# Optimization experiments

Hardware: AMD Instinct MI355X
Metric: run time of the kernel (lower is better)

Reference implementation:

```python
import jax, jax.numpy as jnp
import numpy as np

N_NODES = 50000
N_EDGES = 800000
IN_DIM = 128
HID = 256
OUT = 256


def setup_inputs() -> dict:
    key = jax.random.key(0)
    ks = jax.random.split(key, 16)
    s = 0.05
    return {
        "x": jax.random.normal(ks[0], (N_NODES, IN_DIM), jnp.float32),
        "edge_index": jax.random.randint(ks[1], (2, N_EDGES), 0, N_NODES),
        "W_gcn": jax.random.normal(ks[2], (IN_DIM, HID), jnp.float32) * s,
        "b_gcn": jnp.zeros((HID,), jnp.float32),
        "W_gat": jax.random.normal(ks[3], (IN_DIM, HID), jnp.float32) * s,
        "att_src": jax.random.normal(ks[4], (HID,), jnp.float32) * s,
        "att_dst": jax.random.normal(ks[5], (HID,), jnp.float32) * s,
        "b_gat": jnp.zeros((HID,), jnp.float32),
        "W_sage_l": jax.random.normal(ks[6], (IN_DIM, HID), jnp.float32) * s,
        "b_sage_l": jnp.zeros((HID,), jnp.float32),
        "W_sage_r": jax.random.normal(ks[7], (IN_DIM, HID), jnp.float32) * s,
        "W_fus": jax.random.normal(ks[8], (3 * HID, OUT), jnp.float32) * s,
        "b_fus": jnp.zeros((OUT,), jnp.float32),
    }


def reference(x, edge_index, W_gcn, b_gcn, W_gat, att_src, att_dst, b_gat,
              W_sage_l, b_sage_l, W_sage_r, W_fus, b_fus):
    N = x.shape[0]
    row, col = edge_index[0], edge_index[1]  # source -> target
    loop = jnp.arange(N)
    row_sl = jnp.concatenate([row, loop])  # with self-loops (GCN & GAT)
    col_sl = jnp.concatenate([col, loop])

    # ---- GCNConv: symmetric normalization, transform-then-propagate ----
    xg = x @ W_gcn  # [N, H]
    w = jnp.ones(row_sl.shape[0], x.dtype)
    deg = jax.ops.segment_sum(w, col_sl, num_segments=N)  # >= 1 due to self-loops
    dis = jax.lax.rsqrt(deg)
    norm = dis[row_sl] * dis[col_sl]  # [E+N]
    h_gcn = jax.ops.segment_sum(norm[:, None] * xg[row_sl], col_sl, num_segments=N) + b_gcn

    # ---- GATConv (1 head): attention softmax over incoming edges ----
    xa = x @ W_gat  # [N, H]
    a_src = xa @ att_src  # [N]
    a_dst = xa @ att_dst  # [N]
    e = jax.nn.leaky_relu(a_src[row_sl] + a_dst[col_sl], 0.2)  # [E+N]
    m = jax.ops.segment_max(e, col_sl, num_segments=N)  # per-target max (stable softmax)
    p = jnp.exp(e - m[col_sl])
    z = jax.ops.segment_sum(p, col_sl, num_segments=N)
    alpha = p / (z[col_sl] + 1e-16)
    h_gat = jax.ops.segment_sum(alpha[:, None] * xa[row_sl], col_sl, num_segments=N) + b_gat

    # ---- SAGEConv: mean neighbor aggregation (no self-loops) + root ----
    msum = jax.ops.segment_sum(x[row], col, num_segments=N)
    cnt = jax.ops.segment_sum(jnp.ones(row.shape[0], x.dtype), col, num_segments=N)
    mean = msum / jnp.maximum(cnt, 1.0)[:, None]
    h_sage = mean @ W_sage_l + b_sage_l + x @ W_sage_r

    h = jnp.concatenate([jax.nn.relu(h_gcn), jax.nn.relu(h_gat), jax.nn.relu(h_sage)], axis=1)
    return h @ W_fus + b_fus
```

## Files before the change

### kernel.cpp

```cpp
#include <hip/hip_runtime.h>
#include <hip/hip_bf16.h>

typedef __hip_bfloat16 bf16;
typedef short bf16x8 __attribute__((ext_vector_type(8)));
typedef float f32x4  __attribute__((ext_vector_type(4)));

static constexpr int D_IN  = 128;
static constexpr int D_H   = 256;
static constexpr int D_CAT = 768;

__device__ __forceinline__ float lrelu(float v){ return v > 0.f ? v : 0.2f*v; }
__device__ __forceinline__ bf16  f2b(float v){ return __float2bfloat16(v); }
__device__ __forceinline__ unsigned packb(float lo, float hi){
  bf16 a = f2b(lo), b = f2b(hi);
  unsigned short ua, ub;
  __builtin_memcpy(&ua, &a, 2); __builtin_memcpy(&ub, &b, 2);
  return (unsigned)ua | ((unsigned)ub << 16);
}
__device__ __forceinline__ short bbits(float v){
  bf16 h = f2b(v); short s; __builtin_memcpy(&s, &h, 2); return s;
}
__device__ __forceinline__ unsigned fenc(float f){
  unsigned u = __float_as_uint(f);
  return (u & 0x80000000u) ? ~u : (u | 0x80000000u);
}
__device__ __forceinline__ float fdec(unsigned e){
  unsigned u = (e & 0x80000000u) ? (e ^ 0x80000000u) : ~e;
  return __uint_as_float(u);
}

__device__ __forceinline__ void gload_lds16(const void* g, void* l){
  __builtin_amdgcn_global_load_lds(
      (const __attribute__((address_space(1))) unsigned*)g,
      (__attribute__((address_space(3))) unsigned*)l, 16, 0, 0);
}

__global__ __launch_bounds__(256) void k_prep(
    const float* __restrict__ Wg, const float* __restrict__ Wa,
    const float* __restrict__ Wl, const float* __restrict__ Wr,
    const float* __restrict__ Wf,
    const float* __restrict__ att_src, const float* __restrict__ att_dst,
    const float* __restrict__ bg, const float* __restrict__ ba,
    const float* __restrict__ bs,
    const int* __restrict__ ecol,
    bf16* __restrict__ W1t, bf16* __restrict__ W2t,
    float* __restrict__ bias1, float* __restrict__ wsrc,
    float* __restrict__ wdst, int* __restrict__ cnt, int E)
{
  int b = blockIdx.x, t = threadIdx.x;
  if (b < 768){
    int n = b, k = t;
    float v = 0.f;
    if (n < 256)      { if (k < 128)  v = Wg[(size_t)k*D_H + n]; }
    else if (n < 512) { if (k >= 128) v = Wa[(size_t)(k-128)*D_H + (n-256)]; }
    else              { v = (k < 128) ? Wl[(size_t)k*D_H + (n-512)]
                                      : Wr[(size_t)(k-128)*D_H + (n-512)]; }
    W1t[(size_t)n*256 + k] = f2b(v);
  } else if (b < 1024){
    int n = b - 768;
    for (int k = t; k < D_CAT; k += 256)
      W2t[(size_t)n*D_CAT + k] = f2b(Wf[(size_t)k*D_H + n]);
  } else if (b == 1024){
    bias1[t] = bg[t]; bias1[256+t] = ba[t]; bias1[512+t] = bs[t];
  } else if (b == 1025){
    if (t < 128){
      float s1 = 0.f, s2 = 0.f;
      for (int j = 0; j < D_H; ++j){
        float w = Wa[(size_t)t*D_H + j];
        s1 = fmaf(w, att_src[j], s1);
        s2 = fmaf(w, att_dst[j], s2);
      }
      wsrc[t] = s1; wdst[t] = s2;
    }
  } else {
    int e = (b - 1026)*256 + t;
    if (e < E) atomicAdd(&cnt[ecol[e]], 1);
  }
}

__global__ __launch_bounds__(256) void k_asrc(const float* __restrict__ x,
                                              const float* __restrict__ wsrc,
                                              const float* __restrict__ wdst,
                                              bf16* __restrict__ xb,
                                              float* __restrict__ a_src,
                                              float* __restrict__ a_dst,
                                              unsigned* __restrict__ maxenc,
                                              int N){
  int w = threadIdx.x >> 6, l = threadIdx.x & 63;
  int c = blockIdx.x*4 + w;
  if (c >= N) return;
  float2 xv = *(const float2*)(x + (size_t)c*D_IN + 2*l);
  *(unsigned*)(xb + (size_t)c*D_IN + 2*l) = packb(xv.x, xv.y);
  float s1 = xv.x*wsrc[2*l] + xv.y*wsrc[2*l+1];
  float s2 = xv.x*wdst[2*l] + xv.y*wdst[2*l+1];
  #pragma unroll
  for (int o = 32; o > 0; o >>= 1){
    s1 += __shfl_down(s1, o);
    s2 += __shfl_down(s2, o);
  }
  if (l == 0){ a_src[c] = s1; a_dst[c] = s2; maxenc[c] = fenc(s1); }
}

__global__ __launch_bounds__(256) void k_scanA(const int* __restrict__ cnt,
                                               int* __restrict__ indptr,
                                               int* __restrict__ bsum,
                                               float* __restrict__ dis, int N){
  __shared__ int s[256];
  int t = threadIdx.x, i = blockIdx.x*256 + t;
  int v = (i < N) ? cnt[i] : 0;
  s[t] = v; __syncthreads();
  #pragma unroll
  for (int d = 1; d < 256; d <<= 1){
    int tmp = (t >= d) ? s[t-d] : 0;
    __syncthreads();
    s[t] += tmp;
    __syncthreads();
  }
  if (i < N){
    indptr[i] = s[t] - v;
    dis[i] = rsqrtf((float)v + 1.0f);
  }
  if (t == 255) bsum[blockIdx.x] = s[255];
}

__global__ __launch_bounds__(256) void k_scanB(const int* __restrict__ bsum,
                                               int* __restrict__ boff,
                                               int* __restrict__ indptr,
                                               int nb, int N, int E){
  __shared__ int s[256];
  int t = threadIdx.x;
  int v = (t < nb) ? bsum[t] : 0;
  s[t] = v; __syncthreads();
  #pragma unroll
  for (int d = 1; d < 256; d <<= 1){
    int tmp = (t >= d) ? s[t-d] : 0;
    __syncthreads();
    s[t] += tmp;
    __syncthreads();
  }
  boff[t] = s[t] - v;
  if (t == 0) indptr[N] = E;
}

__global__ __launch_bounds__(256) void k_scanC(int* __restrict__ indptr,
                                               const int* __restrict__ boff, int N){
  int i = blockIdx.x*256 + threadIdx.x;
  if (i < N) indptr[i] += boff[blockIdx.x];
}

__global__ __launch_bounds__(256) void k_fill(const int* __restrict__ row,
                                              const int* __restrict__ col,
                                              const int* __restrict__ indptr,
                                              int* __restrict__ cursor,
                                              int* __restrict__ esrc,
                                              const float* __restrict__ a_src,
                                              unsigned* __restrict__ maxenc,
                                              int E){
  int e = blockIdx.x*256 + threadIdx.x;
  if (e < E){
    int r = row[e], c = col[e];
    int p = indptr[c] + atomicAdd(&cursor[c], 1);
    esrc[p] = r;
    atomicMax(&maxenc[c], fenc(a_src[r]));
  }
}

__global__ __launch_bounds__(256) void k_aggx(
    const int* __restrict__ indptr, const int* __restrict__ esrc,
    const bf16* __restrict__ xb,
    const float* __restrict__ a_src, const float* __restrict__ a_dst,
    const float* __restrict__ dis,
    const unsigned* __restrict__ maxenc,
    bf16* __restrict__ AGG, int N)
{
  int c = blockIdx.x;
  if (c >= N) return;
  int t = threadIdx.x;
  int beg = indptr[c], end = indptr[c+1];
  int deg = end - beg;
  float adst = a_dst[c], dc = dis[c];
  float eself = lrelu(a_src[c] + adst);
  float m = lrelu(fdec(maxenc[c]) + adst);

  __shared__ int   s_src[256];
  __shared__ float s_pe[256];
  __shared__ float s_ds[256];
  __shared__ float pg[4][128], pa[4][128], ps[4][128];
  __shared__ float red[4];

  float p0 = __expf(eself - m);
  float z_loc = (t == 0) ? p0 : 0.f;

  int d2 = t & 63;
  int g  = t >> 6;
  float g0=0.f,g1=0.f,a0=0.f,a1=0.f,sg0=0.f,sg1=0.f;

  for (int ch0 = beg; ch0 < end; ch0 += 256){
    int n = min(256, end - ch0);
    __syncthreads();
    if (t < n){
      int s = esrc[ch0 + t];
      float pe = __expf(lrelu(a_src[s] + adst) - m);
      s_src[t] = s; s_pe[t] = pe; s_ds[t] = dis[s];
      z_loc += pe;
    }
    __syncthreads();
    int i = g;
    for (; i + 28 < n; i += 32){
      unsigned u[8]; float pe[8], ds[8];
      #pragma unroll
      for (int q = 0; q < 8; ++q){
        int s = s_src[i + 4*q];
        u[q] = *(const unsigned*)(xb + (size_t)s*D_IN + 2*d2);
      }
      #pragma unroll
      for (int q = 0; q < 8; ++q){ pe[q] = s_pe[i+4*q]; ds[q] = s_ds[i+4*q]; }
      #pragma unroll
      for (int q = 0; q < 8; ++q){
        float x0 = __uint_as_float(u[q] << 16);
        float x1 = __uint_as_float(u[q] & 0xffff0000u);
        g0 = fmaf(ds[q], x0, g0); g1 = fmaf(ds[q], x1, g1);
        a0 = fmaf(pe[q], x0, a0); a1 = fmaf(pe[q], x1, a1);
        sg0 += x0; sg1 += x1;
      }
    }
    for (; i < n; i += 4){
      int s = s_src[i];
      float pe = s_pe[i], ds = s_ds[i];
      unsigned u = *(const unsigned*)(xb + (size_t)s*D_IN + 2*d2);
      float x0 = __uint_as_float(u << 16);
      float x1 = __uint_as_float(u & 0xffff0000u);
      g0 = fmaf(ds, x0, g0); g1 = fmaf(ds, x1, g1);
      a0 = fmaf(pe, x0, a0); a1 = fmaf(pe, x1, a1);
      sg0 += x0; sg1 += x1;
    }
  }

  #pragma unroll
  for (int o = 32; o > 0; o >>= 1) z_loc += __shfl_down(z_loc, o);
  if ((t & 63) == 0) red[t >> 6] = z_loc;
  __syncthreads();
  float z = red[0] + red[1] + red[2] + red[3];

  pg[g][2*d2] = g0; pg[g][2*d2+1] = g1;
  pa[g][2*d2] = a0; pa[g][2*d2+1] = a1;
  ps[g][2*d2] = sg0; ps[g][2*d2+1] = sg1;
  __syncthreads();

  if (t < 64){
    int d0 = 2*t, d1 = 2*t + 1;
    float G0 = pg[0][d0]+pg[1][d0]+pg[2][d0]+pg[3][d0];
    float G1 = pg[0][d1]+pg[1][d1]+pg[2][d1]+pg[3][d1];
    float A0 = pa[0][d0]+pa[1][d0]+pa[2][d0]+pa[3][d0];
    float A1 = pa[0][d1]+pa[1][d1]+pa[2][d1]+pa[3][d1];
    float S0 = ps[0][d0]+ps[1][d0]+ps[2][d0]+ps[3][d0];
    float S1 = ps[0][d1]+ps[1][d1]+ps[2][d1]+ps[3][d1];
    unsigned xu = *(const unsigned*)(xb + (size_t)c*D_IN + d0);
    float xc0 = __uint_as_float(xu << 16);
    float xc1 = __uint_as_float(xu & 0xffff0000u);
    float invz = 1.f / (z + 1e-16f);
    float invc = 1.f / fmaxf((float)deg, 1.f);
    unsigned* rowp = (unsigned*)(AGG + (size_t)c*512);
    rowp[t]        = packb(dc*(G0 + dc*xc0), dc*(G1 + dc*xc1));
    rowp[64 + t]   = packb((A0 + p0*xc0)*invz, (A1 + p0*xc1)*invz);
    rowp[128 + t]  = packb(S0*invc, S1*invc);
    rowp[192 + t]  = xu;
  }
}

__global__ __launch_bounds__(512, 4) void k_mlp(
    const bf16* __restrict__ AGG,
    const bf16* __restrict__ W1t,
    const bf16* __restrict__ W2t,
    const float* __restrict__ bias1,
    const float* __restrict__ bias2,
    float* __restrict__ out, int M)
{
  __shared__ short A_res[4*64*64];
  __shared__ short Hc[2*64*64];
  __shared__ short SW[256*64];
  int tid  = threadIdx.x;
  int bm   = blockIdx.x*64;
  int wave = tid >> 6, lane = tid & 63;
  int l15  = lane & 15, l4 = lane >> 4;
  int wr   = (wave >> 2)*32;
  int wcol = wave & 3;

  f32x4 oacc[2][4] = {};

  #pragma unroll
  for (int i = 0; i < 4; ++i){
    int slot = i*512 + tid;
    int rr = (slot >> 3) & 63, gp = slot & 7;
    int gk = gp ^ (rr & 7);
    int p  = slot >> 9;
    int row = bm + rr; if (row >= M) row = M - 1;
    gload_lds16(AGG + (size_t)row*512 + p*64 + gk*8, A_res + (size_t)slot*8);
  }

  #pragma unroll
  for (int j = 0; j < 6; ++j){
    if (j == 4){
      #pragma unroll
      for (int i = 0; i < 4; ++i){
        int slot = i*512 + tid;
        int rr = (slot >> 3) & 63, gp = slot & 7;
        int gk = gp ^ (rr & 7);
        int p  = slot >> 9;
        int row = bm + rr; if (row >= M) row = M - 1;
        gload_lds16(AGG + (size_t)row*512 + 256 + p*64 + gk*8, A_res + (size_t)slot*8);
      }
    }
    const int p0 = (j < 2) ? 0 : ((j < 4) ? 2 : 0);
    const int np = (j < 4) ? 2 : 4;
    f32x4 hacc[2][2] = {};
    for (int pp = 0; pp < np; ++pp){
      int p = p0 + pp;
      __syncthreads();
      #pragma unroll
      for (int i = 0; i < 2; ++i){
        int slot = i*512 + tid;
        int r = slot >> 3, gp = slot & 7;
        int gk = gp ^ (r & 7);
        gload_lds16(W1t + (size_t)(j*128 + r)*256 + p*64 + gk*8, SW + (size_t)slot*8);
      }
      __syncthreads();
      #pragma unroll
      for (int kk = 0; kk < 2; ++kk){
        bf16x8 af[2], bfv[2];
        #pragma unroll
        for (int mi = 0; mi < 2; ++mi){
          int r = wr + mi*16 + l15;
          int gk = kk*4 + l4;
          af[mi] = *(const bf16x8*)(A_res + p*4096 + r*64 + ((gk ^ (r & 7))*8));
        }
        #pragma unroll
        for (int ni = 0; ni < 2; ++ni){
          int r = wcol*32 + ni*16 + l15;
          int gk = kk*4 + l4;
          bfv[ni] = *(const bf16x8*)(SW + r*64 + ((gk ^ (r & 7))*8));
        }
        #pragma unroll
        for (int mi = 0; mi < 2; ++mi)
          #pragma unroll
          for (int ni = 0; ni < 2; ++ni)
            hacc[mi][ni] = __builtin_amdgcn_mfma_f32_16x16x32_bf16(
                               af[mi], bfv[ni], hacc[mi][ni], 0, 0, 0);
      }
    }
    #pragma unroll
    for (int mi = 0; mi < 2; ++mi)
      #pragma unroll
      for (int ni = 0; ni < 2; ++ni){
        int cc = wcol*32 + ni*16 + l15;
        float bb = bias1[j*128 + cc];
        int q = cc >> 6, g8 = (cc >> 3) & 7, e = cc & 7;
        #pragma unroll
        for (int r = 0; r < 4; ++r){
          int rr = wr + mi*16 + l4*4 + r;
          float v = fmaxf(hacc[mi][ni][r] + bb, 0.f);
          Hc[q*4096 + rr*64 + ((g8 ^ (rr & 7))*8) + e] = bbits(v);
        }
      }
    #pragma unroll
    for (int q = 0; q < 2; ++q){
      __syncthreads();
      #pragma unroll
      for (int i = 0; i < 4; ++i){
        int slot = i*512 + tid;
        int r = slot >> 3, gp = slot & 7;
        int gk = gp ^ (r & 7);
        gload_lds16(W2t + (size_t)r*768 + j*128 + q*64 + gk*8, SW + (size_t)slot*8);
      }
      __syncthreads();
      #pragma unroll
      for (int kk = 0; kk < 2; ++kk){
        bf16x8 af[2], bfv[4];
        #pragma unroll
        for (int mi = 0; mi < 2; ++mi){
          int r = wr + mi*16 + l15;
          int gk = kk*4 + l4;
          af[mi] = *(const bf16x8*)(Hc + q*4096 + r*64 + ((gk ^ (r & 7))*8));
        }
        #pragma unroll
        for (int ni = 0; ni < 4; ++ni){
          int r = wcol*64 + ni*16 + l15;
          int gk = kk*4 + l4;
          bfv[ni] = *(const bf16x8*)(SW + r*64 + ((gk ^ (r & 7))*8));
        }
        #pragma unroll
        for (int mi = 0; mi < 2; ++mi)
          #pragma unroll
          for (int ni = 0; ni < 4; ++ni)
            oacc[mi][ni] = __builtin_amdgcn_mfma_f32_16x16x32_bf16(
                               af[mi], bfv[ni], oacc[mi][ni], 0, 0, 0);
      }
    }
  }

  #pragma unroll
  for (int mi = 0; mi < 2; ++mi)
    #pragma unroll
    for (int r = 0; r < 4; ++r){
      int row = bm + wr + mi*16 + l4*4 + r;
      if (row >= M) continue;
      #pragma unroll
      for (int ni = 0; ni < 4; ++ni){
        int col = wcol*64 + ni*16 + l15;
        out[(size_t)row*256 + col] = oacc[mi][ni][r] + bias2[col];
      }
    }
}

static inline char* carve(char*& p, size_t bytes){
  char* r = p;
  p += (bytes + 255) & ~(size_t)255;
  return r;
}

extern "C" void kernel_launch(void* const* d_in, const int* in_sizes, int n_in,
                              void* d_out, int out_size, void* d_ws, size_t ws_size,
                              hipStream_t stream) {
  const float* x        = (const float*)d_in[0];
  const int*   ei       = (const int*)  d_in[1];
  const float* W_gcn    = (const float*)d_in[2];
  const float* b_gcn    = (const float*)d_in[3];
  const float* W_gat    = (const float*)d_in[4];
  const float* att_src  = (const float*)d_in[5];
  const float* att_dst  = (const float*)d_in[6];
  const float* b_gat    = (const float*)d_in[7];
  const float* W_sage_l = (const float*)d_in[8];
  const float* b_sage_l = (const float*)d_in[9];
  const float* W_sage_r = (const float*)d_in[10];
  const float* W_fus    = (const float*)d_in[11];
  const float* b_fus    = (const float*)d_in[12];

  const int N = in_sizes[0] / D_IN;
  const int E = in_sizes[1] / 2;
  const int* erow = ei;
  const int* ecol = ei + E;

  char* p = (char*)d_ws;
  bf16*     AGG    = (bf16*)    carve(p, (size_t)N*512*2);
  bf16*     xb     = (bf16*)    carve(p, (size_t)N*D_IN*2);
  bf16*     W1t    = (bf16*)    carve(p, (size_t)D_CAT*256*2);
  bf16*     W2t    = (bf16*)    carve(p, (size_t)256*D_CAT*2);
  float*    bias1  = (float*)   carve(p, D_CAT*4);
  float*    wsrc   = (float*)   carve(p, D_IN*4);
  float*    wdst   = (float*)   carve(p, D_IN*4);
  float*    a_src  = (float*)   carve(p, (size_t)N*4);
  float*    a_dst  = (float*)   carve(p, (size_t)N*4);
  float*    dis    = (float*)   carve(p, (size_t)N*4);
  unsigned* maxenc = (unsigned*)carve(p, (size_t)N*4);
  int*      cnt    = (int*)     carve(p, (size_t)N*4);
  int*      cursor = (int*)     carve(p, (size_t)N*4);
  int*      indptr = (int*)     carve(p, (size_t)(N+1)*4);
  int*      bsum   = (int*)     carve(p, 256*4);
  int*      boff   = (int*)     carve(p, 256*4);
  int*      esrc   = (int*)     carve(p, (size_t)E*4);
  (void)ws_size; (void)n_in; (void)out_size;

  hipMemsetAsync(cnt,    0, (size_t)N*4, stream);
  hipMemsetAsync(cursor, 0, (size_t)N*4, stream);

  const int nb = (N + 255) / 256;
  const int eb = (E + 255) / 256;

  k_prep<<<1026 + eb, 256, 0, stream>>>(W_gcn, W_gat, W_sage_l, W_sage_r, W_fus,
                                        att_src, att_dst, b_gcn, b_gat, b_sage_l,
                                        ecol, W1t, W2t, bias1, wsrc, wdst, cnt, E);

  k_asrc<<<(N + 3)/4, 256, 0, stream>>>(x, wsrc, wdst, xb, a_src, a_dst,
                                        maxenc, N);

  k_scanA<<<nb, 256, 0, stream>>>(cnt, indptr, bsum, dis, N);
  k_scanB<<<1, 256, 0, stream>>>(bsum, boff, indptr, nb, N, E);
  k_scanC<<<nb, 256, 0, stream>>>(indptr, boff, N);
  k_fill <<<eb, 256, 0, stream>>>(erow, ecol, indptr, cursor, esrc,
                                  a_src, maxenc, E);

  k_aggx<<<N, 256, 0, stream>>>(indptr, esrc, xb, a_src, a_dst, dis,
                                maxenc, AGG, N);

  k_mlp<<<(N + 63)/64, 512, 0, stream>>>(AGG, W1t, W2t, bias1, b_fus,
                                         (float*)d_out, N);
}
```

Baseline: 392.8 us.

## Assign one wavefront per target node in aggregation kernel

Measured after the change: 338.2 us. 1.16x faster.

```diff
diff --git a/kernel.cpp b/kernel.cpp
--- a/kernel.cpp
+++ b/kernel.cpp
@@ -173,48 +173,43 @@
     const unsigned* __restrict__ maxenc,
     bf16* __restrict__ AGG, int N)
 {
-  int c = blockIdx.x;
+  int w = threadIdx.x >> 6, l = threadIdx.x & 63;
+  int c = blockIdx.x*4 + w;
   if (c >= N) return;
-  int t = threadIdx.x;
   int beg = indptr[c], end = indptr[c+1];
   int deg = end - beg;
   float adst = a_dst[c], dc = dis[c];
   float eself = lrelu(a_src[c] + adst);
-  float m = lrelu(fdec(maxenc[c]) + adst);
-
-  __shared__ int   s_src[256];
-  __shared__ float s_pe[256];
-  __shared__ float s_ds[256];
-  __shared__ float pg[4][128], pa[4][128], ps[4][128];
-  __shared__ float red[4];
-
+  float m  = lrelu(fdec(maxenc[c]) + adst);
   float p0 = __expf(eself - m);
-  float z_loc = (t == 0) ? p0 : 0.f;
-
-  int d2 = t & 63;
-  int g  = t >> 6;
+
   float g0=0.f,g1=0.f,a0=0.f,a1=0.f,sg0=0.f,sg1=0.f;
-
-  for (int ch0 = beg; ch0 < end; ch0 += 256){
-    int n = min(256, end - ch0);
-    __syncthreads();
-    if (t < n){
-      int s = esrc[ch0 + t];
-      float pe = __expf(lrelu(a_src[s] + adst) - m);
-      s_src[t] = s; s_pe[t] = pe; s_ds[t] = dis[s];
-      z_loc += pe;
-    }
-    __syncthreads();
-    int i = g;
-    for (; i + 28 < n; i += 32){
-      unsigned u[8]; float pe[8], ds[8];
-      #pragma unroll
-      for (int q = 0; q < 8; ++q){
-        int s = s_src[i + 4*q];
-        u[q] = *(const unsigned*)(xb + (size_t)s*D_IN + 2*d2);
-      }
-      #pragma unroll
-      for (int q = 0; q < 8; ++q){ pe[q] = s_pe[i+4*q]; ds[q] = s_ds[i+4*q]; }
+  float z_lane = 0.f;
+
+  for (int ch0 = beg; ch0 < end; ch0 += 64){
+    int cn = min(64, end - ch0);
+    int  idx   = ch0 + ((l < cn) ? l : 0);
+    int  src_l = esrc[idx];
+    float pe_l = 0.f, ds_l = 0.f;
+    if (l < cn){
+      pe_l = __expf(lrelu(a_src[src_l] + adst) - m);
+      ds_l = dis[src_l];
+      z_lane += pe_l;
+    }
+
+    int e = 0;
+    for (; e + 7 < cn; e += 8){
+      int s[8]; unsigned u[8]; float pe[8], ds[8];
+      #pragma unroll
+      for (int q = 0; q < 8; ++q){
+        s[q] = __shfl(src_l, e + q);
+        u[q] = *(const unsigned*)(xb + (size_t)s[q]*D_IN + 2*l);
+      }
+      #pragma unroll
+      for (int q = 0; q < 8; ++q){
+        pe[q] = __shfl(pe_l, e + q);
+        ds[q] = __shfl(ds_l, e + q);
+      }
       #pragma unroll
       for (int q = 0; q < 8; ++q){
         float x0 = __uint_as_float(u[q] << 16);
@@ -224,48 +219,48 @@
         sg0 += x0; sg1 += x1;
       }
     }
-    for (; i < n; i += 4){
-      int s = s_src[i];
-      float pe = s_pe[i], ds = s_ds[i];
-      unsigned u = *(const unsigned*)(xb + (size_t)s*D_IN + 2*d2);
-      float x0 = __uint_as_float(u << 16);
-      float x1 = __uint_as_float(u & 0xffff0000u);
-      g0 = fmaf(ds, x0, g0); g1 = fmaf(ds, x1, g1);
-      a0 = fmaf(pe, x0, a0); a1 = fmaf(pe, x1, a1);
-      sg0 += x0; sg1 += x1;
-    }
-  }
-
-  #pragma unroll
-  for (int o = 32; o > 0; o >>= 1) z_loc += __shfl_down(z_loc, o);
-  if ((t & 63) == 0) red[t >> 6] = z_loc;
-  __syncthreads();
-  float z = red[0] + red[1] + red[2] + red[3];
-
-  pg[g][2*d2] = g0; pg[g][2*d2+1] = g1;
-  pa[g][2*d2] = a0; pa[g][2*d2+1] = a1;
-  ps[g][2*d2] = sg0; ps[g][2*d2+1] = sg1;
-  __syncthreads();
-
-  if (t < 64){
-    int d0 = 2*t, d1 = 2*t + 1;
-    float G0 = pg[0][d0]+pg[1][d0]+pg[2][d0]+pg[3][d0];
-    float G1 = pg[0][d1]+pg[1][d1]+pg[2][d1]+pg[3][d1];
-    float A0 = pa[0][d0]+pa[1][d0]+pa[2][d0]+pa[3][d0];
-    float A1 = pa[0][d1]+pa[1][d1]+pa[2][d1]+pa[3][d1];
-    float S0 = ps[0][d0]+ps[1][d0]+ps[2][d0]+ps[3][d0];
-    float S1 = ps[0][d1]+ps[1][d1]+ps[2][d1]+ps[3][d1];
-    unsigned xu = *(const unsigned*)(xb + (size_t)c*D_IN + d0);
-    float xc0 = __uint_as_float(xu << 16);
-    float xc1 = __uint_as_float(xu & 0xffff0000u);
-    float invz = 1.f / (z + 1e-16f);
-    float invc = 1.f / fmaxf((float)deg, 1.f);
-    unsigned* rowp = (unsigned*)(AGG + (size_t)c*512);
-    rowp[t]        = packb(dc*(G0 + dc*xc0), dc*(G1 + dc*xc1));
-    rowp[64 + t]   = packb((A0 + p0*xc0)*invz, (A1 + p0*xc1)*invz);
-    rowp[128 + t]  = packb(S0*invc, S1*invc);
-    rowp[192 + t]  = xu;
-  }
+    if (e < cn){
+      int s[8]; unsigned u[8]; float pe[8], ds[8], mk[8];
+      #pragma unroll
+      for (int q = 0; q < 8; ++q){
+        int ee = e + q; ee = (ee < cn) ? ee : (cn - 1);
+        s[q] = __shfl(src_l, ee);
+        u[q] = *(const unsigned*)(xb + (size_t)s[q]*D_IN + 2*l);
+      }
+      #pragma unroll
+      for (int q = 0; q < 8; ++q){
+        bool v = (e + q) < cn;
+        int ee = v ? (e + q) : 63;
+        pe[q] = __shfl(pe_l, ee);
+        ds[q] = __shfl(ds_l, ee);
+        mk[q] = v ? 1.f : 0.f;
+      }
+      #pragma unroll
+      for (int q = 0; q < 8; ++q){
+        float x0 = __uint_as_float(u[q] << 16);
+        float x1 = __uint_as_float(u[q] & 0xffff0000u);
+        g0 = fmaf(ds[q], x0, g0); g1 = fmaf(ds[q], x1, g1);
+        a0 = fmaf(pe[q], x0, a0); a1 = fmaf(pe[q], x1, a1);
+        sg0 = fmaf(mk[q], x0, sg0); sg1 = fmaf(mk[q], x1, sg1);
+      }
+    }
+  }
+
+  float z = z_lane;
+  #pragma unroll
+  for (int o = 32; o > 0; o >>= 1) z += __shfl_down(z, o);
+  z = __shfl(z, 0) + p0;
+
+  unsigned xu = *(const unsigned*)(xb + (size_t)c*D_IN + 2*l);
+  float xc0 = __uint_as_float(xu << 16);
+  float xc1 = __uint_as_float(xu & 0xffff0000u);
+  float invz = 1.f / (z + 1e-16f);
+  float invc = 1.f / fmaxf((float)deg, 1.f);
+  unsigned* rowp = (unsigned*)(AGG + (size_t)c*512);
+  rowp[l]       = packb(dc*(g0 + dc*xc0), dc*(g1 + dc*xc1));
+  rowp[64 + l]  = packb((a0 + p0*xc0)*invz, (a1 + p0*xc1)*invz);
+  rowp[128 + l] = packb(sg0*invc, sg1*invc);
+  rowp[192 + l] = xu;
 }
 
 __global__ __launch_bounds__(512, 4) void k_mlp(
@@ -479,8 +474,8 @@
   k_fill <<<eb, 256, 0, stream>>>(erow, ecol, indptr, cursor, esrc,
                                   a_src, maxenc, E);
 
-  k_aggx<<<N, 256, 0, stream>>>(indptr, esrc, xb, a_src, a_dst, dis,
-                                maxenc, AGG, N);
+  k_aggx<<<(N + 3)/4, 256, 0, stream>>>(indptr, esrc, xb, a_src, a_dst, dis,
+                                        maxenc, AGG, N);
 
   k_mlp<<<(N + 63)/64, 512, 0, stream>>>(AGG, W1t, W2t, bias1, b_fus,
                                          (float*)d_out, N);
```
